# Kernel tuning notes

Hardware: AMD Instinct MI355X
Metric: run time of the kernel (lower is better)

The kernel has to match this reference:

```python
import jax, jax.numpy as jnp
import numpy as np

D, N, L, H, VOCAB = 256, 8192, 6, 4, 256
EPS = 1e-5


def layernorm(x):
    # LayerNorm over last dim, no affine (matches nn.LayerNorm(D, elementwise_affine=False))
    mu = jnp.mean(x, axis=-1, keepdims=True)
    var = jnp.mean(jnp.square(x - mu), axis=-1, keepdims=True)
    return (x - mu) * jax.lax.rsqrt(var + EPS)


def rotate_half(x):
    x1, x2 = jnp.split(x, 2, axis=-1)
    return jnp.concatenate((-x2, x1), axis=-1)


def rope_tables(T, dim, dtype):
    inv_freq = 1.0 / (10000.0 ** (jnp.arange(0, dim, 2, dtype=jnp.float32) / dim))
    t = jnp.arange(T, dtype=jnp.float32)
    freqs = jnp.einsum('i,j->ij', t, inv_freq)          # [T, dim/2]
    emb = jnp.concatenate((freqs, freqs), axis=-1)       # [T, dim]
    return jnp.cos(emb).astype(dtype), jnp.sin(emb).astype(dtype)


def linear_attention(Q, K, V):
    # unnormalized causal attention with RoPE on Q, K
    B, T, d = Q.shape
    cos, sin = rope_tables(T, d, Q.dtype)
    Qr = Q * cos + rotate_half(Q) * sin
    Kr = K * cos + rotate_half(K) * sin
    energy = jnp.einsum('btd,bsd->bts', Qr, Kr)          # [B, T, T]
    mask = jnp.tril(jnp.ones((T, T), dtype=energy.dtype))
    energy = energy * mask
    return jnp.einsum('bts,bsd->btd', energy, V)


def setup_inputs() -> dict:
    key = jax.random.key(0)
    ks = jax.random.split(key, 6)
    idx = jax.random.randint(ks[0], (4, 2048), 0, VOCAB)
    wte = jax.random.normal(ks[1], (VOCAB, D), dtype=jnp.float32) * 0.02
    encoder = jax.random.normal(ks[2], (N, D), dtype=jnp.float32) * 0.02
    decoder_x = jax.random.normal(ks[3], (H, D, N // H), dtype=jnp.float32) * 0.02
    decoder_y = jax.random.normal(ks[4], (H, D, N // H), dtype=jnp.float32) * 0.02
    readout = jax.random.normal(ks[5], (D, VOCAB), dtype=jnp.float32) * 0.02
    return {"idx": idx, "wte": wte, "encoder": encoder,
            "decoder_x": decoder_x, "decoder_y": decoder_y, "readout": readout}


def reference(idx, wte, encoder, decoder_x, decoder_y, readout):
    B, T = idx.shape
    v_ast = layernorm(wte[idx])                          # [B, T, D]
    for _ in range(L):
        x_raw = jnp.einsum('btd,hdm->bthm', v_ast, decoder_x)
        x = jax.nn.relu(x_raw)                           # [B, T, H, N/H]
        a_ast = linear_attention(v_ast, v_ast, v_ast)
        y_raw = jnp.einsum('btd,hdm->bthm', layernorm(a_ast), decoder_y)
        y = jax.nn.relu(y_raw) * x
        y_flat = y.reshape(B, T, -1)                     # [B, T, N]
        update = y_flat @ encoder                        # [B, T, D]
        v_ast = v_ast + layernorm(update)
    logits = v_ast @ readout                             # [B, T, VOCAB]
    return logits
```

## Files before the change

kernel.cpp:

```cpp
#include <hip/hip_runtime.h>
#include <hip/hip_bf16.h>

typedef __hip_bfloat16 bf16;
typedef _Float16 half_t;
typedef __attribute__((ext_vector_type(8))) _Float16 half8;
typedef __attribute__((ext_vector_type(4))) float f32x4;

#define LN_EPS 1e-5f

static constexpr int Dk     = 256;
static constexpr int Tk     = 2048;
static constexpr int BTk    = 8192;
static constexpr int MHk    = 2048;
static constexpr int Nk     = 8192;
static constexpr int LAYERS = 6;
static constexpr long long TD  = (long long)Tk * Dk;
static constexpr long long BTD = (long long)BTk * Dk;
static constexpr long long TT  = (long long)Tk * Tk;

__device__ __forceinline__ float wave_reduce(float v) {
#pragma unroll
    for (int o = 32; o > 0; o >>= 1) v += __shfl_down(v, o);
    return v;
}

__device__ __forceinline__ float block_sum_256(float x, float* sbuf) {
    float s = wave_reduce(x);
    int lane = threadIdx.x & 63, wv = threadIdx.x >> 6;
    if (lane == 0) sbuf[wv] = s;
    __syncthreads();
    float r = sbuf[0] + sbuf[1] + sbuf[2] + sbuf[3];
    __syncthreads();
    return r;
}

__device__ __forceinline__ void glds16(const void* g, void* lds) {
    __builtin_amdgcn_global_load_lds(
        (const __attribute__((address_space(1))) void*)g,
        (__attribute__((address_space(3))) void*)lds, 16, 0, 0);
}

__global__ __launch_bounds__(256) void sniff_kernel(const unsigned short* __restrict__ w,
                                                    int* __restrict__ flag) {
    __shared__ float sbuf[4];
    int tid = threadIdx.x;
    float cnt = 0.f;
    for (int i = tid; i < 1024; i += 256) {
        int e = (w[i] >> 7) & 0xFF;
        if (e >= 128) cnt += 1.f;
    }
    float tot = block_sum_256(cnt, sbuf);
    if (tid == 0) *flag = (tot > 32.f) ? 1 : 0;
}

__global__ __launch_bounds__(256) void tr_cvt16_kernel(const void* __restrict__ src,
                                                       const int* __restrict__ flag,
                                                       half_t* __restrict__ dst,
                                                       int R, int C,
                                                       long long sz, long long dz) {
    __shared__ float t[32][33];
    bool f32 = (*flag != 0);
    int ct = blockIdx.x * 32, rt = blockIdx.y * 32;
    long long so = (long long)blockIdx.z * sz, dofs = (long long)blockIdx.z * dz;
    int tx = threadIdx.x & 31, ty = threadIdx.x >> 5;
#pragma unroll
    for (int i = 0; i < 4; i++) {
        long long idx = so + (long long)(rt + ty + i * 8) * C + ct + tx;
        t[ty + i * 8][tx] = f32 ? ((const float*)src)[idx] : (float)((const bf16*)src)[idx];
    }
    __syncthreads();
#pragma unroll
    for (int i = 0; i < 4; i++) {
        long long odx = dofs + (long long)(ct + ty + i * 8) * R + rt + tx;
        dst[odx] = (half_t)t[tx][ty + i * 8];
    }
}

__global__ __launch_bounds__(256) void trv_kernel(const float* __restrict__ src,
                                                  half_t* __restrict__ dst) {
    __shared__ float t[32][33];
    int ct = blockIdx.x * 32, rt = blockIdx.y * 32;
    int tx = threadIdx.x & 31, ty = threadIdx.x >> 5;
#pragma unroll
    for (int i = 0; i < 4; i++)
        t[ty + i * 8][tx] = src[(long long)(rt + ty + i * 8) * Dk + ct + tx];
    __syncthreads();
#pragma unroll
    for (int i = 0; i < 4; i++)
        dst[(long long)(ct + ty + i * 8) * BTk + rt + tx] = (half_t)t[tx][ty + i * 8];
}

__global__ __launch_bounds__(256) void embed_ln_kernel(const int* __restrict__ idx,
                                                       const void* __restrict__ wte,
                                                       const int* __restrict__ flag,
                                                       float* __restrict__ v,
                                                       half_t* __restrict__ vf) {
    __shared__ float sbuf[4];
    int bt = blockIdx.x, tid = threadIdx.x;
    int id = idx[bt];
    bool f32 = (*flag != 0);
    float x = f32 ? ((const float*)wte)[id * Dk + tid]
                  : (float)((const bf16*)wte)[id * Dk + tid];
    float mu = block_sum_256(x, sbuf) * (1.f / 256.f);
    float d = x - mu;
    float var = block_sum_256(d * d, sbuf) * (1.f / 256.f);
    float r = d * rsqrtf(var + LN_EPS);
    v[bt * Dk + tid] = r;
    vf[bt * Dk + tid] = (half_t)r;
}

__global__ __launch_bounds__(256) void ln_rows_kernel(const float* __restrict__ Pa,
                                                      half_t* __restrict__ of) {
    __shared__ float sbuf[4];
    int bt = blockIdx.x, tid = threadIdx.x;
    int b = bt >> 11, t = bt & (Tk - 1);
    int ncnt = ((t & ~127) >> 9) + 1;
    const float* p = Pa + ((long long)(b << 2)) * TD + (long long)t * Dk + tid;
    float x = 0.f;
    for (int c = 0; c < ncnt; c++) x += p[(long long)c * TD];
    float mu = block_sum_256(x, sbuf) * (1.f / 256.f);
    float d = x - mu;
    float var = block_sum_256(d * d, sbuf) * (1.f / 256.f);
    float r = d * rsqrtf(var + LN_EPS);
    of[bt * Dk + tid] = (half_t)r;
}

__global__ __launch_bounds__(256) void add_ln_kernel(const float* __restrict__ Pu,
                                                     float* __restrict__ v,
                                                     half_t* __restrict__ vf) {
    __shared__ float sbuf[4];
    int bt = blockIdx.x, tid = threadIdx.x;
    long long e = (long long)bt * Dk + tid;
    float x = Pu[e] + Pu[e + BTD] + Pu[e + 2 * BTD] + Pu[e + 3 * BTD];
    float mu = block_sum_256(x, sbuf) * (1.f / 256.f);
    float d = x - mu;
    float var = block_sum_256(d * d, sbuf) * (1.f / 256.f);
    float r = d * rsqrtf(var + LN_EPS);
    float nv = v[e] + r;
    v[e] = nv;
    vf[e] = (half_t)nv;
}

__global__ __launch_bounds__(128) void rope_kernel(const float* __restrict__ v,
                                                   half_t* __restrict__ qf) {
    int bt = blockIdx.x, i = threadIdx.x;
    int t = bt & (Tk - 1);
    float invf = powf(10000.f, -(float)i / 128.f);
    float ang = (float)t * invf;
    float s, c;
    sincosf(ang, &s, &c);
    float q1 = v[bt * Dk + i];
    float q2 = v[bt * Dk + 128 + i];
    qf[bt * Dk + i]       = (half_t)(q1 * c - q2 * s);
    qf[bt * Dk + 128 + i] = (half_t)(q2 * c + q1 * s);
}

__global__ __launch_bounds__(256) void gemm128e(
    const half_t* __restrict__ Q, half_t* __restrict__ E) {
    __shared__ __align__(16) half_t As[128 * 32];
    __shared__ __align__(16) half_t Bs[128 * 32];
    const int tid = threadIdx.x;
    const int lane = tid & 63, wv = tid >> 6;
    const int wr = wv >> 1, wc = wv & 1;
    const int quad = lane >> 4, r = lane & 15;
    const int mb = blockIdx.y * 128, nb = blockIdx.x * 128;
    const half_t* Qb = Q + (long long)blockIdx.z * TD;
    half_t* Eb = E + (long long)blockIdx.z * TT;

    if ((int)blockIdx.x > (int)blockIdx.y) {
#pragma unroll
        for (int e = 0; e < 64; e++) {
            int ii = e * 256 + tid;
            Eb[(long long)(mb + (ii >> 7)) * Tk + nb + (ii & 127)] = (half_t)0.f;
        }
        return;
    }

    f32x4 acc[4][4] = {};
    const int srow = tid >> 2, skq = (tid & 3) * 8;
    const int wbase = (tid & 192) * 8;
    for (int k0 = 0; k0 < Dk; k0 += 32) {
#pragma unroll
        for (int rnd = 0; rnd < 2; rnd++) {
            int row = rnd * 64 + srow;
            glds16(Qb + (long long)(mb + row) * Dk + k0 + skq, As + rnd * 2048 + wbase);
            glds16(Qb + (long long)(nb + row) * Dk + k0 + skq, Bs + rnd * 2048 + wbase);
        }
        __syncthreads();
        half8 bfr[4];
#pragma unroll
        for (int ni = 0; ni < 4; ni++)
            bfr[ni] = *(const half8*)&Bs[(wc * 64 + ni * 16 + r) * 32 + quad * 8];
#pragma unroll
        for (int mi = 0; mi < 4; mi++) {
            half8 afr = *(const half8*)&As[(wr * 64 + mi * 16 + r) * 32 + quad * 8];
#pragma unroll
            for (int ni = 0; ni < 4; ni++)
                acc[mi][ni] = __builtin_amdgcn_mfma_f32_16x16x32_f16(afr, bfr[ni], acc[mi][ni], 0, 0, 0);
        }
        __syncthreads();
    }
#pragma unroll
    for (int mi = 0; mi < 4; mi++)
#pragma unroll
        for (int ni = 0; ni < 4; ni++) {
            int row0 = mb + wr * 64 + mi * 16 + quad * 4;
            int col = nb + wc * 64 + ni * 16 + r;
#pragma unroll
            for (int rr = 0; rr < 4; rr++) {
                int row = row0 + rr;
                float val = (row < col) ? 0.f : acc[mi][ni][rr];
                Eb[(long long)row * Tk + col] = (half_t)val;
            }
        }
}

__global__ __launch_bounds__(256) void gemm128a(
    const half_t* __restrict__ E, const half_t* __restrict__ vT,
    float* __restrict__ Pa) {
    __shared__ __align__(16) half_t As[128 * 32];
    __shared__ __align__(16) half_t Bs[128 * 32];
    const int tid = threadIdx.x;
    const int lane = tid & 63, wv = tid >> 6;
    const int wr = wv >> 1, wc = wv & 1;
    const int quad = lane >> 4, r = lane & 15;
    const int mb = blockIdx.y * 128, nb = blockIdx.x * 128;
    const int b = blockIdx.z >> 2, c = blockIdx.z & 3;
    const int kbeg = c * 512;
    const int kend = min(mb + 128, kbeg + 512);
    if (kend <= kbeg) return;

    const half_t* Ab = E + (long long)b * TT;
    const half_t* Bb = vT + (long long)b * Tk;
    float* Pc = Pa + (long long)blockIdx.z * TD;
    f32x4 acc[4][4] = {};
    const int srow = tid >> 2, skq = (tid & 3) * 8;
    const int wbase = (tid & 192) * 8;
    for (int k0 = kbeg; k0 < kend; k0 += 32) {
#pragma unroll
        for (int rnd = 0; rnd < 2; rnd++) {
            int row = rnd * 64 + srow;
            glds16(Ab + (long long)(mb + row) * Tk + k0 + skq, As + rnd * 2048 + wbase);
            glds16(Bb + (long long)(nb + row) * BTk + k0 + skq, Bs + rnd * 2048 + wbase);
        }
        __syncthreads();
        half8 bfr[4];
#pragma unroll
        for (int ni = 0; ni < 4; ni++)
            bfr[ni] = *(const half8*)&Bs[(wc * 64 + ni * 16 + r) * 32 + quad * 8];
#pragma unroll
        for (int mi = 0; mi < 4; mi++) {
            half8 afr = *(const half8*)&As[(wr * 64 + mi * 16 + r) * 32 + quad * 8];
#pragma unroll
            for (int ni = 0; ni < 4; ni++)
                acc[mi][ni] = __builtin_amdgcn_mfma_f32_16x16x32_f16(afr, bfr[ni], acc[mi][ni], 0, 0, 0);
        }
        __syncthreads();
    }
#pragma unroll
    for (int mi = 0; mi < 4; mi++)
#pragma unroll
        for (int ni = 0; ni < 4; ni++) {
            int row0 = mb + wr * 64 + mi * 16 + quad * 4;
            int col = nb + wc * 64 + ni * 16 + r;
#pragma unroll
            for (int rr = 0; rr < 4; rr++)
                Pc[(long long)(row0 + rr) * Dk + col] = acc[mi][ni][rr];
        }
}

__global__ __launch_bounds__(512) void dual_gemm(
    const half_t* __restrict__ A1,
    const half_t* __restrict__ A2,
    const half_t* __restrict__ dxT,
    const half_t* __restrict__ dyT,
    half_t* __restrict__ C) {
    __shared__ __align__(16) half_t As1[128 * 32];
    __shared__ __align__(16) half_t As2[128 * 32];
    __shared__ __align__(16) half_t Bs1[128 * 32];
    __shared__ __align__(16) half_t Bs2[128 * 32];
    const int tid = threadIdx.x;
    const int lane = tid & 63, wv = tid >> 6;
    const int wr = wv >> 2, wc = wv & 3;
    const int quad = lane >> 4, r = lane & 15;
    const int mb = blockIdx.y * 128, nb = blockIdx.x * 128;
    const int h = blockIdx.z;
    const half_t* B1 = dxT + (long long)h * MHk * Dk;
    const half_t* B2 = dyT + (long long)h * MHk * Dk;

    f32x4 accX[4][2] = {};
    f32x4 accY[4][2] = {};
    const int srow = tid >> 2, skq = (tid & 3) * 8;
    const int wbase = (tid & 448) * 8;
    for (int k0 = 0; k0 < Dk; k0 += 32) {
        glds16(A1 + (long long)(mb + srow) * Dk + k0 + skq, As1 + wbase);
        glds16(A2 + (long long)(mb + srow) * Dk + k0 + skq, As2 + wbase);
        glds16(B1 + (long long)(nb + srow) * Dk + k0 + skq, Bs1 + wbase);
        glds16(B2 + (long long)(nb + srow) * Dk + k0 + skq, Bs2 + wbase);
        __syncthreads();
        half8 b1f[2], b2f[2];
#pragma unroll
        for (int ni = 0; ni < 2; ni++) {
            b1f[ni] = *(const half8*)&Bs1[(wc * 32 + ni * 16 + r) * 32 + quad * 8];
            b2f[ni] = *(const half8*)&Bs2[(wc * 32 + ni * 16 + r) * 32 + quad * 8];
        }
#pragma unroll
        for (int mi = 0; mi < 4; mi++) {
            half8 a1 = *(const half8*)&As1[(wr * 64 + mi * 16 + r) * 32 + quad * 8];
            half8 a2 = *(const half8*)&As2[(wr * 64 + mi * 16 + r) * 32 + quad * 8];
#pragma unroll
            for (int ni = 0; ni < 2; ni++) {
                accX[mi][ni] = __builtin_amdgcn_mfma_f32_16x16x32_f16(a1, b1f[ni], accX[mi][ni], 0, 0, 0);
                accY[mi][ni] = __builtin_amdgcn_mfma_f32_16x16x32_f16(a2, b2f[ni], accY[mi][ni], 0, 0, 0);
            }
        }
        __syncthreads();
    }
#pragma unroll
    for (int mi = 0; mi < 4; mi++)
#pragma unroll
        for (int ni = 0; ni < 2; ni++) {
            int row0 = mb + wr * 64 + mi * 16 + quad * 4;
            int col = h * MHk + nb + wc * 32 + ni * 16 + r;
#pragma unroll
            for (int rr = 0; rr < 4; rr++) {
                float val = fmaxf(accY[mi][ni][rr], 0.f) * fmaxf(accX[mi][ni][rr], 0.f);
                C[(long long)(row0 + rr) * Nk + col] = (half_t)val;
            }
        }
}

__global__ __launch_bounds__(256) void gemm128u(
    const half_t* __restrict__ A, const half_t* __restrict__ B,
    float* __restrict__ Pu) {
    __shared__ __align__(16) half_t As[128 * 32];
    __shared__ __align__(16) half_t Bs[128 * 32];
    const int tid = threadIdx.x;
    const int lane = tid & 63, wv = tid >> 6;
    const int wr = wv >> 1, wc = wv & 1;
    const int quad = lane >> 4, r = lane & 15;
    const int mb = blockIdx.y * 128, nb = blockIdx.x * 128;
    const int kbeg = blockIdx.z * 2048;
    float* Pc = Pu + (long long)blockIdx.z * BTD;

    f32x4 acc[4][4] = {};
    const int srow = tid >> 2, skq = (tid & 3) * 8;
    const int wbase = (tid & 192) * 8;
    for (int k0 = kbeg; k0 < kbeg + 2048; k0 += 32) {
#pragma unroll
        for (int rnd = 0; rnd < 2; rnd++) {
            int row = rnd * 64 + srow;
            glds16(A + (long long)(mb + row) * Nk + k0 + skq, As + rnd * 2048 + wbase);
            glds16(B + (long long)(nb + row) * Nk + k0 + skq, Bs + rnd * 2048 + wbase);
        }
        __syncthreads();
        half8 bfr[4];
#pragma unroll
        for (int ni = 0; ni < 4; ni++)
            bfr[ni] = *(const half8*)&Bs[(wc * 64 + ni * 16 + r) * 32 + quad * 8];
#pragma unroll
        for (int mi = 0; mi < 4; mi++) {
            half8 afr = *(const half8*)&As[(wr * 64 + mi * 16 + r) * 32 + quad * 8];
#pragma unroll
            for (int ni = 0; ni < 4; ni++)
                acc[mi][ni] = __builtin_amdgcn_mfma_f32_16x16x32_f16(afr, bfr[ni], acc[mi][ni], 0, 0, 0);
        }
        __syncthreads();
    }
#pragma unroll
    for (int mi = 0; mi < 4; mi++)
#pragma unroll
        for (int ni = 0; ni < 4; ni++) {
            int row0 = mb + wr * 64 + mi * 16 + quad * 4;
            int col = nb + wc * 64 + ni * 16 + r;
#pragma unroll
            for (int rr = 0; rr < 4; rr++)
                Pc[(long long)(row0 + rr) * Dk + col] = acc[mi][ni][rr];
        }
}

__global__ __launch_bounds__(256) void gemm64h(
    const half_t* __restrict__ A, int lda,
    const half_t* __restrict__ B, int ldb,
    float* __restrict__ C, int ldc, int K) {
    __shared__ __align__(16) half_t As[64 * 32];
    __shared__ __align__(16) half_t Bs[64 * 32];
    const int tid = threadIdx.x;
    const int lane = tid & 63, wv = tid >> 6;
    const int wr = wv >> 1, wc = wv & 1;
    const int quad = lane >> 4, r = lane & 15;
    const int mb = blockIdx.y * 64, nb = blockIdx.x * 64;

    f32x4 acc[2][2] = {};
    const int srow = tid >> 2, skq = (tid & 3) * 8;
    const int wbase = (tid & 192) * 8;
    for (int k0 = 0; k0 < K; k0 += 32) {
        glds16(A + (long long)(mb + srow) * lda + k0 + skq, As + wbase);
        glds16(B + (long long)(nb + srow) * ldb + k0 + skq, Bs + wbase);
        __syncthreads();
        half8 b0 = *(const half8*)&Bs[(wc * 32 +  0 + r) * 32 + quad * 8];
        half8 b1 = *(const half8*)&Bs[(wc * 32 + 16 + r) * 32 + quad * 8];
#pragma unroll
        for (int mi = 0; mi < 2; mi++) {
            half8 afr = *(const half8*)&As[(wr * 32 + mi * 16 + r) * 32 + quad * 8];
            acc[mi][0] = __builtin_amdgcn_mfma_f32_16x16x32_f16(afr, b0, acc[mi][0], 0, 0, 0);
            acc[mi][1] = __builtin_amdgcn_mfma_f32_16x16x32_f16(afr, b1, acc[mi][1], 0, 0, 0);
        }
        __syncthreads();
    }
#pragma unroll
    for (int mi = 0; mi < 2; mi++)
#pragma unroll
        for (int ni = 0; ni < 2; ni++) {
            int row0 = mb + wr * 32 + mi * 16 + quad * 4;
            int col = nb + wc * 32 + ni * 16 + r;
#pragma unroll
            for (int rr = 0; rr < 4; rr++)
                C[(long long)(row0 + rr) * ldc + col] = acc[mi][ni][rr];
        }
}

extern "C" void kernel_launch(void* const* d_in, const int* in_sizes, int n_in,
                              void* d_out, int out_size, void* d_ws, size_t ws_size,
                              hipStream_t stream) {
    (void)in_sizes; (void)n_in; (void)out_size; (void)ws_size;
    const int* idx = (const int*)d_in[0];
    float* out = (float*)d_out;

    char* ws = (char*)d_ws;
    float*  v32  = (float*) (ws);
    half_t* vf   = (half_t*)(ws + (  8ll << 20));
    half_t* qf   = (half_t*)(ws + ( 12ll << 20));
    half_t* vT   = (half_t*)(ws + ( 16ll << 20));
    half_t* lnf  = (half_t*)(ws + ( 20ll << 20));
    half_t* E    = (half_t*)(ws + ( 24ll << 20));
    float*  Pa   = (float*) (ws + ( 56ll << 20));
    float*  Pu   = (float*) (ws + ( 24ll << 20));
    half_t* y16  = (half_t*)(ws + ( 88ll << 20));
    half_t* dxT  = (half_t*)(ws + (216ll << 20));
    half_t* dyT  = (half_t*)(ws + (220ll << 20));
    half_t* eT   = (half_t*)(ws + (224ll << 20));
    half_t* roT  = (half_t*)(ws + (228ll << 20));
    int*    flag = (int*)   (ws + (228ll << 20) + (256ll << 10));

    sniff_kernel<<<1, 256, 0, stream>>>((const unsigned short*)d_in[1], flag);
    tr_cvt16_kernel<<<dim3(MHk / 32, Dk / 32, 4), 256, 0, stream>>>(
        d_in[3], flag, dxT, Dk, MHk, (long long)Dk * MHk, (long long)Dk * MHk);
    tr_cvt16_kernel<<<dim3(MHk / 32, Dk / 32, 4), 256, 0, stream>>>(
        d_in[4], flag, dyT, Dk, MHk, (long long)Dk * MHk, (long long)Dk * MHk);
    tr_cvt16_kernel<<<dim3(Dk / 32, Nk / 32, 1), 256, 0, stream>>>(
        d_in[2], flag, eT, Nk, Dk, 0, 0);
    tr_cvt16_kernel<<<dim3(Dk / 32, Dk / 32, 1), 256, 0, stream>>>(
        d_in[5], flag, roT, Dk, Dk, 0, 0);

    embed_ln_kernel<<<BTk, 256, 0, stream>>>(idx, d_in[1], flag, v32, vf);

    for (int l = 0; l < LAYERS; l++) {
        rope_kernel<<<BTk, 128, 0, stream>>>(v32, qf);
        trv_kernel<<<dim3(Dk / 32, BTk / 32), 256, 0, stream>>>(v32, vT);
        gemm128e<<<dim3(Tk / 128, Tk / 128, 4), 256, 0, stream>>>(qf, E);
        gemm128a<<<dim3(Dk / 128, Tk / 128, 16), 256, 0, stream>>>(E, vT, Pa);
        ln_rows_kernel<<<BTk, 256, 0, stream>>>(Pa, lnf);
        dual_gemm<<<dim3(MHk / 128, BTk / 128, 4), 512, 0, stream>>>(
            vf, lnf, dxT, dyT, y16);
        gemm128u<<<dim3(Dk / 128, BTk / 128, 4), 256, 0, stream>>>(y16, eT, Pu);
        add_ln_kernel<<<BTk, 256, 0, stream>>>(Pu, v32, vf);
    }
    gemm64h<<<dim3(Dk / 64, BTk / 64), 256, 0, stream>>>(
        vf, Dk, roT, Dk, out, Dk, Dk);
}
```

Baseline: 1.468 ms.

## Chunk dual-gemm/encoder GEMM per head and XOR-swizzle LDS layouts

Splits the y computation and the encoder GEMM into four per-head chunks that reuse a 2048-column y buffer, so the intermediate is smaller and more likely to stay in cache instead of round-tripping a full 8192-wide tensor. Each chunk's encoder GEMM uses 128x64 tiles with a 2-way K split, producing 8 partial sums that add_ln now reduces. An XOR swizzle is also added to the LDS writes and fragment reads of all MFMA GEMMs to cut bank conflicts. The cost is more kernel launches, more partial-sum traffic in add_ln, and smaller tiles in the encoder GEMM.

```diff
diff --git a/kernel.cpp b/kernel.cpp
--- a/kernel.cpp
+++ b/kernel.cpp
@@ -13,10 +13,13 @@
 static constexpr int BTk    = 8192;
 static constexpr int MHk    = 2048;
 static constexpr int Nk     = 8192;
+static constexpr int CH     = 2048;
 static constexpr int LAYERS = 6;
 static constexpr long long TD  = (long long)Tk * Dk;
 static constexpr long long BTD = (long long)BTk * Dk;
 static constexpr long long TT  = (long long)Tk * Tk;
+
+#define SKQ(t) ((((t) & 3) ^ (((t) >> 3) & 3)) * 8)
 
 __device__ __forceinline__ float wave_reduce(float v) {
 #pragma unroll
@@ -131,7 +134,9 @@
     __shared__ float sbuf[4];
     int bt = blockIdx.x, tid = threadIdx.x;
     long long e = (long long)bt * Dk + tid;
-    float x = Pu[e] + Pu[e + BTD] + Pu[e + 2 * BTD] + Pu[e + 3 * BTD];
+    float x = 0.f;
+#pragma unroll
+    for (int p = 0; p < 8; p++) x += Pu[e + (long long)p * BTD];
     float mu = block_sum_256(x, sbuf) * (1.f / 256.f);
     float d = x - mu;
     float var = block_sum_256(d * d, sbuf) * (1.f / 256.f);
@@ -163,6 +168,7 @@
     const int lane = tid & 63, wv = tid >> 6;
     const int wr = wv >> 1, wc = wv & 1;
     const int quad = lane >> 4, r = lane & 15;
+    const int qsw = (quad ^ ((r >> 1) & 3)) * 8;
     const int mb = blockIdx.y * 128, nb = blockIdx.x * 128;
     const half_t* Qb = Q + (long long)blockIdx.z * TD;
     half_t* Eb = E + (long long)blockIdx.z * TT;
@@ -177,7 +183,7 @@
     }
 
     f32x4 acc[4][4] = {};
-    const int srow = tid >> 2, skq = (tid & 3) * 8;
+    const int srow = tid >> 2, skq = SKQ(tid);
     const int wbase = (tid & 192) * 8;
     for (int k0 = 0; k0 < Dk; k0 += 32) {
 #pragma unroll
@@ -190,10 +196,10 @@
         half8 bfr[4];
 #pragma unroll
         for (int ni = 0; ni < 4; ni++)
-            bfr[ni] = *(const half8*)&Bs[(wc * 64 + ni * 16 + r) * 32 + quad * 8];
+            bfr[ni] = *(const half8*)&Bs[(wc * 64 + ni * 16 + r) * 32 + qsw];
 #pragma unroll
         for (int mi = 0; mi < 4; mi++) {
-            half8 afr = *(const half8*)&As[(wr * 64 + mi * 16 + r) * 32 + quad * 8];
+            half8 afr = *(const half8*)&As[(wr * 64 + mi * 16 + r) * 32 + qsw];
 #pragma unroll
             for (int ni = 0; ni < 4; ni++)
                 acc[mi][ni] = __builtin_amdgcn_mfma_f32_16x16x32_f16(afr, bfr[ni], acc[mi][ni], 0, 0, 0);
@@ -224,6 +230,7 @@
     const int lane = tid & 63, wv = tid >> 6;
     const int wr = wv >> 1, wc = wv & 1;
     const int quad = lane >> 4, r = lane & 15;
+    const int qsw = (quad ^ ((r >> 1) & 3)) * 8;
     const int mb = blockIdx.y * 128, nb = blockIdx.x * 128;
     const int b = blockIdx.z >> 2, c = blockIdx.z & 3;
     const int kbeg = c * 512;
@@ -234,7 +241,7 @@
     const half_t* Bb = vT + (long long)b * Tk;
     float* Pc = Pa + (long long)blockIdx.z * TD;
     f32x4 acc[4][4] = {};
-    const int srow = tid >> 2, skq = (tid & 3) * 8;
+    const int srow = tid >> 2, skq = SKQ(tid);
     const int wbase = (tid & 192) * 8;
     for (int k0 = kbeg; k0 < kend; k0 += 32) {
 #pragma unroll
@@ -247,10 +254,10 @@
         half8 bfr[4];
 #pragma unroll
         for (int ni = 0; ni < 4; ni++)
-            bfr[ni] = *(const half8*)&Bs[(wc * 64 + ni * 16 + r) * 32 + quad * 8];
+            bfr[ni] = *(const half8*)&Bs[(wc * 64 + ni * 16 + r) * 32 + qsw];
 #pragma unroll
         for (int mi = 0; mi < 4; mi++) {
-            half8 afr = *(const half8*)&As[(wr * 64 + mi * 16 + r) * 32 + quad * 8];
+            half8 afr = *(const half8*)&As[(wr * 64 + mi * 16 + r) * 32 + qsw];
 #pragma unroll
             for (int ni = 0; ni < 4; ni++)
                 acc[mi][ni] = __builtin_amdgcn_mfma_f32_16x16x32_f16(afr, bfr[ni], acc[mi][ni], 0, 0, 0);
@@ -269,11 +276,11 @@
         }
 }
 
-__global__ __launch_bounds__(512) void dual_gemm(
+__global__ __launch_bounds__(512) void dual_gemm_c(
     const half_t* __restrict__ A1,
     const half_t* __restrict__ A2,
-    const half_t* __restrict__ dxT,
-    const half_t* __restrict__ dyT,
+    const half_t* __restrict__ B1,
+    const half_t* __restrict__ B2,
     half_t* __restrict__ C) {
     __shared__ __align__(16) half_t As1[128 * 32];
     __shared__ __align__(16) half_t As2[128 * 32];
@@ -283,14 +290,12 @@
     const int lane = tid & 63, wv = tid >> 6;
     const int wr = wv >> 2, wc = wv & 3;
     const int quad = lane >> 4, r = lane & 15;
+    const int qsw = (quad ^ ((r >> 1) & 3)) * 8;
     const int mb = blockIdx.y * 128, nb = blockIdx.x * 128;
-    const int h = blockIdx.z;
-    const half_t* B1 = dxT + (long long)h * MHk * Dk;
-    const half_t* B2 = dyT + (long long)h * MHk * Dk;
 
     f32x4 accX[4][2] = {};
     f32x4 accY[4][2] = {};
-    const int srow = tid >> 2, skq = (tid & 3) * 8;
+    const int srow = tid >> 2, skq = SKQ(tid);
     const int wbase = (tid & 448) * 8;
     for (int k0 = 0; k0 < Dk; k0 += 32) {
         glds16(A1 + (long long)(mb + srow) * Dk + k0 + skq, As1 + wbase);
@@ -301,13 +306,13 @@
         half8 b1f[2], b2f[2];
 #pragma unroll
         for (int ni = 0; ni < 2; ni++) {
-            b1f[ni] = *(const half8*)&Bs1[(wc * 32 + ni * 16 + r) * 32 + quad * 8];
-            b2f[ni] = *(const half8*)&Bs2[(wc * 32 + ni * 16 + r) * 32 + quad * 8];
+            b1f[ni] = *(const half8*)&Bs1[(wc * 32 + ni * 16 + r) * 32 + qsw];
+            b2f[ni] = *(const half8*)&Bs2[(wc * 32 + ni * 16 + r) * 32 + qsw];
         }
 #pragma unroll
         for (int mi = 0; mi < 4; mi++) {
-            half8 a1 = *(const half8*)&As1[(wr * 64 + mi * 16 + r) * 32 + quad * 8];
-            half8 a2 = *(const half8*)&As2[(wr * 64 + mi * 16 + r) * 32 + quad * 8];
+            half8 a1 = *(const half8*)&As1[(wr * 64 + mi * 16 + r) * 32 + qsw];
+            half8 a2 = *(const half8*)&As2[(wr * 64 + mi * 16 + r) * 32 + qsw];
 #pragma unroll
             for (int ni = 0; ni < 2; ni++) {
                 accX[mi][ni] = __builtin_amdgcn_mfma_f32_16x16x32_f16(a1, b1f[ni], accX[mi][ni], 0, 0, 0);
@@ -321,48 +326,49 @@
 #pragma unroll
         for (int ni = 0; ni < 2; ni++) {
             int row0 = mb + wr * 64 + mi * 16 + quad * 4;
-            int col = h * MHk + nb + wc * 32 + ni * 16 + r;
+            int col = nb + wc * 32 + ni * 16 + r;
 #pragma unroll
             for (int rr = 0; rr < 4; rr++) {
                 float val = fmaxf(accY[mi][ni][rr], 0.f) * fmaxf(accX[mi][ni][rr], 0.f);
-                C[(long long)(row0 + rr) * Nk + col] = (half_t)val;
+                C[(long long)(row0 + rr) * CH + col] = (half_t)val;
             }
         }
 }
 
-__global__ __launch_bounds__(256) void gemm128u(
+__global__ __launch_bounds__(256) void gemm128u_c(
     const half_t* __restrict__ A, const half_t* __restrict__ B,
     float* __restrict__ Pu) {
     __shared__ __align__(16) half_t As[128 * 32];
-    __shared__ __align__(16) half_t Bs[128 * 32];
+    __shared__ __align__(16) half_t Bs[64 * 32];
     const int tid = threadIdx.x;
     const int lane = tid & 63, wv = tid >> 6;
     const int wr = wv >> 1, wc = wv & 1;
     const int quad = lane >> 4, r = lane & 15;
-    const int mb = blockIdx.y * 128, nb = blockIdx.x * 128;
-    const int kbeg = blockIdx.z * 2048;
+    const int qsw = (quad ^ ((r >> 1) & 3)) * 8;
+    const int mb = blockIdx.y * 128, nb = blockIdx.x * 64;
+    const int kbeg = blockIdx.z * (CH / 2);
     float* Pc = Pu + (long long)blockIdx.z * BTD;
 
-    f32x4 acc[4][4] = {};
-    const int srow = tid >> 2, skq = (tid & 3) * 8;
+    f32x4 acc[4][2] = {};
+    const int srow = tid >> 2, skq = SKQ(tid);
     const int wbase = (tid & 192) * 8;
-    for (int k0 = kbeg; k0 < kbeg + 2048; k0 += 32) {
+    for (int k0 = kbeg; k0 < kbeg + CH / 2; k0 += 32) {
 #pragma unroll
         for (int rnd = 0; rnd < 2; rnd++) {
             int row = rnd * 64 + srow;
-            glds16(A + (long long)(mb + row) * Nk + k0 + skq, As + rnd * 2048 + wbase);
-            glds16(B + (long long)(nb + row) * Nk + k0 + skq, Bs + rnd * 2048 + wbase);
-        }
-        __syncthreads();
-        half8 bfr[4];
-#pragma unroll
-        for (int ni = 0; ni < 4; ni++)
-            bfr[ni] = *(const half8*)&Bs[(wc * 64 + ni * 16 + r) * 32 + quad * 8];
+            glds16(A + (long long)(mb + row) * CH + k0 + skq, As + rnd * 2048 + wbase);
+        }
+        glds16(B + (long long)(nb + srow) * Nk + k0 + skq, Bs + wbase);
+        __syncthreads();
+        half8 bfr[2];
+#pragma unroll
+        for (int ni = 0; ni < 2; ni++)
+            bfr[ni] = *(const half8*)&Bs[(wc * 32 + ni * 16 + r) * 32 + qsw];
 #pragma unroll
         for (int mi = 0; mi < 4; mi++) {
-            half8 afr = *(const half8*)&As[(wr * 64 + mi * 16 + r) * 32 + quad * 8];
-#pragma unroll
-            for (int ni = 0; ni < 4; ni++)
+            half8 afr = *(const half8*)&As[(wr * 64 + mi * 16 + r) * 32 + qsw];
+#pragma unroll
+            for (int ni = 0; ni < 2; ni++)
                 acc[mi][ni] = __builtin_amdgcn_mfma_f32_16x16x32_f16(afr, bfr[ni], acc[mi][ni], 0, 0, 0);
         }
         __syncthreads();
@@ -370,9 +376,9 @@
 #pragma unroll
     for (int mi = 0; mi < 4; mi++)
 #pragma unroll
-        for (int ni = 0; ni < 4; ni++) {
+        for (int ni = 0; ni < 2; ni++) {
             int row0 = mb + wr * 64 + mi * 16 + quad * 4;
-            int col = nb + wc * 64 + ni * 16 + r;
+            int col = nb + wc * 32 + ni * 16 + r;
 #pragma unroll
             for (int rr = 0; rr < 4; rr++)
                 Pc[(long long)(row0 + rr) * Dk + col] = acc[mi][ni][rr];
@@ -436,12 +442,12 @@
     half_t* E    = (half_t*)(ws + ( 24ll << 20));
     float*  Pa   = (float*) (ws + ( 56ll << 20));
     float*  Pu   = (float*) (ws + ( 24ll << 20));
-    half_t* y16  = (half_t*)(ws + ( 88ll << 20));
-    half_t* dxT  = (half_t*)(ws + (216ll << 20));
-    half_t* dyT  = (half_t*)(ws + (220ll << 20));
-    half_t* eT   = (half_t*)(ws + (224ll << 20));
-    half_t* roT  = (half_t*)(ws + (228ll << 20));
-    int*    flag = (int*)   (ws + (228ll << 20) + (256ll << 10));
+    half_t* yc   = (half_t*)(ws + ( 88ll << 20));
+    half_t* dxT  = (half_t*)(ws + (120ll << 20));
+    half_t* dyT  = (half_t*)(ws + (124ll << 20));
+    half_t* eT   = (half_t*)(ws + (128ll << 20));
+    half_t* roT  = (half_t*)(ws + (132ll << 20));
+    int*    flag = (int*)   (ws + (132ll << 20) + (256ll << 10));
 
     sniff_kernel<<<1, 256, 0, stream>>>((const unsigned short*)d_in[1], flag);
     tr_cvt16_kernel<<<dim3(MHk / 32, Dk / 32, 4), 256, 0, stream>>>(
@@ -461,9 +467,12 @@
         gemm128e<<<dim3(Tk / 128, Tk / 128, 4), 256, 0, stream>>>(qf, E);
         gemm128a<<<dim3(Dk / 128, Tk / 128, 16), 256, 0, stream>>>(E, vT, Pa);
         ln_rows_kernel<<<BTk, 256, 0, stream>>>(Pa, lnf);
-        dual_gemm<<<dim3(MHk / 128, BTk / 128, 4), 512, 0, stream>>>(
-            vf, lnf, dxT, dyT, y16);
-        gemm128u<<<dim3(Dk / 128, BTk / 128, 4), 256, 0, stream>>>(y16, eT, Pu);
+        for (int c = 0; c < 4; c++) {
+            dual_gemm_c<<<dim3(CH / 128, BTk / 128), 512, 0, stream>>>(
+                vf, lnf, dxT + (long long)c * CH * Dk, dyT + (long long)c * CH * Dk, yc);
+            gemm128u_c<<<dim3(Dk / 64, BTk / 128, 2), 256, 0, stream>>>(
+                yc, eT + (long long)c * CH, Pu + (long long)c * 2 * BTD);
+        }
         add_ln_kernel<<<BTk, 256, 0, stream>>>(Pu, v32, vf);
     }
     gemm64h<<<dim3(Dk / 64, BTk / 64), 256, 0, stream>>>(
```

New measurement: 1.799 ms. +22.6%, slower.
